# Optimization experiments

Hardware: AMD Instinct MI355X
Metric: run time of the kernel (lower is better)

The kernel has to match this reference:

```python
import jax, jax.numpy as jnp
import numpy as np

N = 40000; E = 500000; IN = 128; ED = 16; HID = 64; HEADS = 4; OUT = 256; B = 128
NEG = 0.2  # GATv2 leaky_relu negative slope


def _add_self_loops(edge_index, edge_attr, n):
    # PyG add_self_loops with fill_value='mean': loop attr = mean of incoming edge attrs per node
    dst = edge_index[1]
    s = jax.ops.segment_sum(edge_attr, dst, num_segments=n)
    c = jax.ops.segment_sum(jnp.ones((edge_attr.shape[0],), edge_attr.dtype), dst, num_segments=n)
    loop_attr = s / jnp.maximum(c, 1.0)[:, None]
    loops = jnp.arange(n, dtype=edge_index.dtype)
    ei = jnp.concatenate([edge_index, jnp.stack([loops, loops])], axis=1)
    ea = jnp.concatenate([edge_attr, loop_attr], axis=0)
    return ei, ea


def _seg_softmax(logits, seg, n):
    m = jax.ops.segment_max(logits, seg, num_segments=n)
    m = jnp.where(jnp.isfinite(m), m, 0.0)  # guard empty segments
    e = jnp.exp(logits - m[seg])
    z = jax.ops.segment_sum(e, seg, num_segments=n)
    return e / (z[seg] + 1e-16)


def _gatv2(x, src, dst, ea, Wl, bl, Wr, br, We, att, bias, heads, oc, concat):
    n = x.shape[0]
    xl = (x @ Wl + bl).reshape(n, heads, oc)  # lin_l (source/message transform)
    xr = (x @ Wr + br).reshape(n, heads, oc)  # lin_r (target transform)
    ef = (ea @ We).reshape(-1, heads, oc)     # lin_edge (no bias)
    s = jax.nn.leaky_relu(xl[src] + xr[dst] + ef, NEG)  # [Etot,H,C]
    alpha = _seg_softmax(jnp.einsum('ehc,hc->eh', s, att), dst, n)  # scatter-softmax over dst
    out = jax.ops.segment_sum(xl[src] * alpha[..., None], dst, num_segments=n)  # [N,H,C]
    out = out.reshape(n, heads * oc) if concat else out.mean(axis=1)
    return out + bias


def setup_inputs():
    ks = jax.random.split(jax.random.key(0), 32)
    W = lambda i, shp: jax.random.normal(ks[i], shp, jnp.float32) * 0.05
    z = lambda d: jnp.zeros((d,), jnp.float32)
    H = HEADS * HID
    return dict(
        x=jax.random.normal(ks[0], (N, IN), jnp.float32),
        edge_index=jax.random.randint(ks[1], (2, E), 0, N),
        edge_attr=jax.random.normal(ks[2], (E, ED), jnp.float32),
        batch=jnp.sort(jax.random.randint(ks[3], (N,), 0, B)),
        batch_size=B,
        c1_Wl=W(4, (IN, H)), c1_bl=z(H), c1_Wr=W(5, (IN, H)), c1_br=z(H), c1_We=W(6, (ED, H)), c1_att=W(7, (HEADS, HID)), c1_bias=z(H),
        c2_Wl=W(8, (H, H)), c2_bl=z(H), c2_Wr=W(9, (H, H)), c2_br=z(H), c2_We=W(10, (ED, H)), c2_att=W(11, (HEADS, HID)), c2_bias=z(H),
        c3_Wl=W(12, (H, OUT)), c3_bl=z(OUT), c3_Wr=W(13, (H, OUT)), c3_br=z(OUT), c3_We=W(14, (ED, OUT)), c3_att=W(15, (1, OUT)), c3_bias=z(OUT),
        gate_W1=W(16, (OUT, 128)), gate_b1=z(128), gate_W2=W(17, (128, 1)), gate_b2=z(1),
        reg_W1=W(18, (OUT, 128)), reg_b1=z(128), reg_W2=W(19, (128, 2)), reg_b2=z(2),
    )


def reference(x, edge_index, edge_attr, batch, batch_size,
              c1_Wl, c1_bl, c1_Wr, c1_br, c1_We, c1_att, c1_bias,
              c2_Wl, c2_bl, c2_Wr, c2_br, c2_We, c2_att, c2_bias,
              c3_Wl, c3_bl, c3_Wr, c3_br, c3_We, c3_att, c3_bias,
              gate_W1, gate_b1, gate_W2, gate_b2,
              reg_W1, reg_b1, reg_W2, reg_b2):
    # task_type='homo_lumo' path; dropout disabled (inference)
    ei, ea = _add_self_loops(edge_index, edge_attr, N)
    src, dst = ei[0], ei[1]
    h = jax.nn.relu(_gatv2(x, src, dst, ea, c1_Wl, c1_bl, c1_Wr, c1_br, c1_We, c1_att, c1_bias, HEADS, HID, True))
    h = jax.nn.relu(_gatv2(h, src, dst, ea, c2_Wl, c2_bl, c2_Wr, c2_br, c2_We, c2_att, c2_bias, HEADS, HID, True))
    h = _gatv2(h, src, dst, ea, c3_Wl, c3_bl, c3_Wr, c3_br, c3_We, c3_att, c3_bias, 1, OUT, True)
    # AttentionalAggregation pooling
    gate = jax.nn.relu(h @ gate_W1 + gate_b1) @ gate_W2 + gate_b2  # [N,1]
    a = _seg_softmax(gate[:, 0], batch, batch_size)
    g = jax.ops.segment_sum(h * a[:, None], batch, num_segments=batch_size)  # [B,OUT]
    return jax.nn.relu(g @ reg_W1 + reg_b1) @ reg_W2 + reg_b2  # [B,2]
```

## Files before the change

kernel.cpp:

```cpp
#include <hip/hip_runtime.h>
#include <math.h>

constexpr int N_NODES = 40000;
constexpr int N_EDGES = 500000;
constexpr int ETOT    = N_EDGES + N_NODES;
constexpr int IN_DIM  = 128;
constexpr int ED_DIM  = 16;
constexpr int FEAT    = 256;
constexpr int BATCH   = 128;
constexpr float NEG   = 0.2f;
constexpr int NCHUNK  = (N_NODES + 255) / 256;

__global__ __launch_bounds__(256) void k_deg(const int* __restrict__ dst, int* __restrict__ deg)
{
    int e = blockIdx.x * 256 + threadIdx.x;
    if (e >= ETOT) return;
    int v = e < N_EDGES ? dst[e] : e - N_EDGES;
    atomicAdd(&deg[v], 1);
}

__global__ __launch_bounds__(256) void k_scan1(const int* __restrict__ deg, int* __restrict__ bsum)
{
    __shared__ int s[256];
    int t = threadIdx.x;
    int idx = blockIdx.x * 256 + t;
    s[t] = idx < N_NODES ? deg[idx] : 0;
    __syncthreads();
    for (int st = 128; st; st >>= 1) { if (t < st) s[t] += s[t + st]; __syncthreads(); }
    if (t == 0) bsum[blockIdx.x] = s[0];
}

__global__ __launch_bounds__(256) void k_scan2(const int* __restrict__ bsum,
    int* __restrict__ boff, int* __restrict__ rowptr)
{
    __shared__ int s[256];
    int t = threadIdx.x;
    int v = t < NCHUNK ? bsum[t] : 0;
    s[t] = v;
    __syncthreads();
    for (int off = 1; off < 256; off <<= 1) {
        int x = (t >= off) ? s[t - off] : 0;
        __syncthreads();
        s[t] += x;
        __syncthreads();
    }
    if (t < NCHUNK) boff[t] = s[t] - v;
    if (t == 0) rowptr[N_NODES] = ETOT;
}

__global__ __launch_bounds__(256) void k_scan3(const int* __restrict__ deg,
    const int* __restrict__ boff, int* __restrict__ rowptr)
{
    __shared__ int s[256];
    int t = threadIdx.x;
    int idx = blockIdx.x * 256 + t;
    int v = idx < N_NODES ? deg[idx] : 0;
    s[t] = v;
    __syncthreads();
    for (int off = 1; off < 256; off <<= 1) {
        int x = (t >= off) ? s[t - off] : 0;
        __syncthreads();
        s[t] += x;
        __syncthreads();
    }
    if (idx < N_NODES) rowptr[idx] = boff[blockIdx.x] + s[t] - v;
}

__global__ __launch_bounds__(256) void k_fill(const int* __restrict__ srcA, const int* __restrict__ dst,
    const int* __restrict__ rowptr, int* __restrict__ fill, int2* __restrict__ elist2)
{
    int e = blockIdx.x * 256 + threadIdx.x;
    if (e >= ETOT) return;
    int v = e < N_EDGES ? dst[e]  : e - N_EDGES;
    int s = e < N_EDGES ? srcA[e] : e - N_EDGES;
    int pos = rowptr[v] + atomicAdd(&fill[v], 1);
    elist2[pos] = make_int2(s, e);
}

__global__ __launch_bounds__(256) void k_loop_csr(const int2* __restrict__ elist2,
    const int* __restrict__ rowptr, const float* __restrict__ ea, float* __restrict__ loop_attr)
{
    int t = blockIdx.x * 256 + threadIdx.x;
    if (t >= N_NODES * ED_DIM) return;
    int n = t >> 4, d = t & 15;
    int p0 = rowptr[n], p1 = rowptr[n + 1];
    float s = 0.f; int c = 0;
    for (int p = p0; p < p1; ++p) {
        int e = elist2[p].y;
        if (e < N_EDGES) { s += ea[(size_t)e * ED_DIM + d]; ++c; }
    }
    loop_attr[t] = s / (float)(c > 0 ? c : 1);
}

__global__ __launch_bounds__(256) void k_gemm(const float* __restrict__ A, const float* __restrict__ W,
    const float* __restrict__ bias, float* __restrict__ C, int M, int N, int K, int act)
{
    __shared__ float As[16][136];
    __shared__ float Bs[16][136];
    int t = threadIdx.x;
    int bm = blockIdx.x * 128, bn = blockIdx.y * 128;
    int tr = t >> 4, tc = t & 15;
    int mr0 = tr * 8, nc0 = tc * 4;

    float acc[8][8] = {};

    for (int k0 = 0; k0 < K; k0 += 16) {
        #pragma unroll
        for (int ii = 0; ii < 2; ++ii) {
            int i = t + ii * 256;
            int row = i >> 2, kq = (i & 3) << 2;
            int r = bm + row; r = r < M ? r : M - 1;
            float4 av = *(const float4*)(A + (size_t)r * K + k0 + kq);
            As[kq + 0][row] = av.x; As[kq + 1][row] = av.y;
            As[kq + 2][row] = av.z; As[kq + 3][row] = av.w;
        }
        #pragma unroll
        for (int ii = 0; ii < 2; ++ii) {
            int i = t + ii * 256;
            int krow = i >> 5, nq = (i & 31) << 2;
            float4 bv = *(const float4*)(W + (size_t)(k0 + krow) * N + bn + nq);
            *(float4*)&Bs[krow][nq] = bv;
        }
        __syncthreads();
        #pragma unroll
        for (int k = 0; k < 16; ++k) {
            float4 a0 = *(const float4*)&As[k][mr0];
            float4 a1 = *(const float4*)&As[k][mr0 + 4];
            float4 b0 = *(const float4*)&Bs[k][nc0];
            float4 b1 = *(const float4*)&Bs[k][64 + nc0];
            float am[8] = {a0.x, a0.y, a0.z, a0.w, a1.x, a1.y, a1.z, a1.w};
            float bv[8] = {b0.x, b0.y, b0.z, b0.w, b1.x, b1.y, b1.z, b1.w};
            #pragma unroll
            for (int i = 0; i < 8; ++i)
                #pragma unroll
                for (int j = 0; j < 8; ++j)
                    acc[i][j] = fmaf(am[i], bv[j], acc[i][j]);
        }
        __syncthreads();
    }

    float bb[8];
    #pragma unroll
    for (int j = 0; j < 4; ++j) { bb[j] = bias[bn + nc0 + j]; bb[j + 4] = bias[bn + 64 + nc0 + j]; }
    #pragma unroll
    for (int i = 0; i < 8; ++i) {
        int row = bm + mr0 + i;
        if (row >= M) break;
        float4 o0, o1;
        o0.x = acc[i][0] + bb[0]; o0.y = acc[i][1] + bb[1];
        o0.z = acc[i][2] + bb[2]; o0.w = acc[i][3] + bb[3];
        o1.x = acc[i][4] + bb[4]; o1.y = acc[i][5] + bb[5];
        o1.z = acc[i][6] + bb[6]; o1.w = acc[i][7] + bb[7];
        if (act) {
            o0.x = fmaxf(o0.x, 0.f); o0.y = fmaxf(o0.y, 0.f); o0.z = fmaxf(o0.z, 0.f); o0.w = fmaxf(o0.w, 0.f);
            o1.x = fmaxf(o1.x, 0.f); o1.y = fmaxf(o1.y, 0.f); o1.z = fmaxf(o1.z, 0.f); o1.w = fmaxf(o1.w, 0.f);
        }
        *(float4*)(C + (size_t)row * N + bn + nc0)      = o0;
        *(float4*)(C + (size_t)row * N + bn + 64 + nc0) = o1;
    }
}

static void launch_gemm(const float* A, const float* W, const float* bias, float* C,
                        int M, int N, int K, int act, hipStream_t stream)
{
    dim3 grid((M + 127) / 128, N / 128);
    k_gemm<<<grid, 256, 0, stream>>>(A, W, bias, C, M, N, K, act);
}


#define XELOAD(s) do {                                                                \
    int src_ = eS[s].x, e_ = eS[s].y;                                                 \
    const float4* eb4_ = reinterpret_cast<const float4*>(                             \
        (e_ < N_EDGES) ? ea + (size_t)e_ * ED_DIM                                     \
                       : loop_attr + (size_t)src_ * ED_DIM);                          \
    evS[s][0] = eb4_[0]; evS[s][1] = eb4_[1];                                         \
    evS[s][2] = eb4_[2]; evS[s][3] = eb4_[3];                                         \
    const float* xp_ = xl + (size_t)src_ * FEAT + base;                               \
    xlvS[s][0] = xp_[0];  xlvS[s][1] = xp_[16];                                       \
    xlvS[s][2] = xp_[32]; xlvS[s][3] = xp_[48];                                       \
} while (0)

#define COMPUTE(s) do {                                                               \
    float ef0_ = 0.f, ef1_ = 0.f, ef2_ = 0.f, ef3_ = 0.f;                             \
    const float* ed_ = (const float*)evS[s];                                          \
    _Pragma("unroll")                                                                 \
    for (int d_ = 0; d_ < ED_DIM; ++d_) {                                             \
        float a_ = ed_[d_];                                                           \
        ef0_ = fmaf(a_, weR[d_][0], ef0_); ef1_ = fmaf(a_, weR[d_][1], ef1_);         \
        ef2_ = fmaf(a_, weR[d_][2], ef2_); ef3_ = fmaf(a_, weR[d_][3], ef3_);         \
    }                                                                                 \
    float s0_ = xlvS[s][0] + xrv[0] + ef0_;                                           \
    float s1_ = xlvS[s][1] + xrv[1] + ef1_;                                           \
    float s2_ = xlvS[s][2] + xrv[2] + ef2_;                                           \
    float s3_ = xlvS[s][3] + xrv[3] + ef3_;                                           \
    s0_ = fmaxf(s0_, 0.f) + NEG * fminf(s0_, 0.f);                                    \
    s1_ = fmaxf(s1_, 0.f) + NEG * fminf(s1_, 0.f);                                    \
    s2_ = fmaxf(s2_, 0.f) + NEG * fminf(s2_, 0.f);                                    \
    s3_ = fmaxf(s3_, 0.f) + NEG * fminf(s3_, 0.f);                                    \
    float l_ = fmaf(s0_, attR[0], fmaf(s1_, attR[1], fmaf(s2_, attR[2], s3_ * attR[3])));\
    l_ += __shfl_xor(l_, 1, 64);                                                      \
    l_ += __shfl_xor(l_, 2, 64);                                                      \
    l_ += __shfl_xor(l_, 4, 64);                                                      \
    l_ += __shfl_xor(l_, 8, 64);                                                      \
    if (H == 1) { l_ += __shfl_xor(l_, 16, 64); l_ += __shfl_xor(l_, 32, 64); }       \
    float nm_ = fmaxf(m, l_);                                                         \
    float sc_ = __expf(m - nm_);                                                      \
    float w_  = __expf(l_ - nm_);                                                     \
    z = fmaf(z, sc_, w_);                                                             \
    m = nm_;                                                                          \
    acc[0] = fmaf(acc[0], sc_, w_ * xlvS[s][0]);                                      \
    acc[1] = fmaf(acc[1], sc_, w_ * xlvS[s][1]);                                      \
    acc[2] = fmaf(acc[2], sc_, w_ * xlvS[s][2]);                                      \
    acc[3] = fmaf(acc[3], sc_, w_ * xlvS[s][3]);                                      \
} while (0)

template <int H, int RELU>
__global__ __launch_bounds__(256, 3) void k_gat(
    const float* __restrict__ xl, const float* __restrict__ xr,
    const float* __restrict__ ea, const float* __restrict__ loop_attr,
    const int2* __restrict__ elist2, const int* __restrict__ rowptr,
    const float* __restrict__ We, const float* __restrict__ att,
    const float* __restrict__ bias, float* __restrict__ out)
{
    int t = threadIdx.x;
    int lane = t & 63;
    int n = __builtin_amdgcn_readfirstlane(blockIdx.x * 4 + (t >> 6));
    int q = lane >> 4;
    int u = lane & 15;
    int base = q * 64 + u;

    float weR[ED_DIM][4];
    #pragma unroll
    for (int d = 0; d < ED_DIM; ++d) {
        #pragma unroll
        for (int j = 0; j < 4; ++j) weR[d][j] = We[d * FEAT + base + 16 * j];
    }
    #pragma unroll
    for (int d = 0; d < ED_DIM; ++d) {
        #pragma unroll
        for (int j = 0; j < 4; ++j) asm volatile("" : "+v"(weR[d][j]));
    }

    float attR[4], xrv[4];
    #pragma unroll
    for (int j = 0; j < 4; ++j) {
        attR[j] = att[base + 16 * j];
        xrv[j]  = xr[(size_t)n * FEAT + base + 16 * j];
    }

    float m = -INFINITY, z = 0.f;
    float acc[4] = {0.f, 0.f, 0.f, 0.f};

    int p0 = rowptr[n], p1 = rowptr[n + 1];
    int pe = p1 - 1;

    int2   eS[2];
    float4 evS[2][4];
    float  xlvS[2][4];

    eS[0] = elist2[p0];
    { int pc = p0 + 1 > pe ? pe : p0 + 1; eS[1] = elist2[pc]; }
    XELOAD(0);

    int p = p0;
    while (true) {
        XELOAD(1);
        { int pn = p + 2 > pe ? pe : p + 2; eS[0] = elist2[pn]; }
        COMPUTE(0);
        if (++p >= p1) break;
        XELOAD(0);
        { int pn = p + 2 > pe ? pe : p + 2; eS[1] = elist2[pn]; }
        COMPUTE(1);
        if (++p >= p1) break;
    }

    float inv = 1.0f / (z + 1e-16f);
    #pragma unroll
    for (int j = 0; j < 4; ++j) {
        float o = fmaf(acc[j], inv, bias[base + 16 * j]);
        if (RELU) o = fmaxf(o, 0.f);
        out[(size_t)n * FEAT + base + 16 * j] = o;
    }
}

__global__ __launch_bounds__(256) void k_gate_score(const float* __restrict__ ghid,
    const float* __restrict__ W2, const float* __restrict__ b2, float* __restrict__ gate)
{
    int lane = threadIdx.x & 63;
    int n = blockIdx.x * 4 + (threadIdx.x >> 6);
    float v = ghid[(size_t)n * 128 + lane] * W2[lane] + ghid[(size_t)n * 128 + lane + 64] * W2[lane + 64];
    #pragma unroll
    for (int off = 32; off > 0; off >>= 1) v += __shfl_xor(v, off, 64);
    if (lane == 0) gate[n] = v + b2[0];
}

__device__ __forceinline__ int lbound(const int* a, int n, int v)
{
    int lo = 0, hi = n;
    while (lo < hi) { int mid = (lo + hi) >> 1; if (a[mid] < v) lo = mid + 1; else hi = mid; }
    return lo;
}

__global__ __launch_bounds__(256) void k_pool(const float* __restrict__ gate,
    const float* __restrict__ h, const int* __restrict__ batch, float* __restrict__ g)
{
    int b = blockIdx.x;
    int t = threadIdx.x;
    __shared__ float red[256];
    int start = lbound(batch, N_NODES, b);
    int end   = lbound(batch, N_NODES, b + 1);

    float mx = -INFINITY;
    for (int n = start + t; n < end; n += 256) mx = fmaxf(mx, gate[n]);
    red[t] = mx; __syncthreads();
    for (int s = 128; s; s >>= 1) { if (t < s) red[t] = fmaxf(red[t], red[t + s]); __syncthreads(); }
    float m = red[0];
    __syncthreads();

    float zs = 0.f;
    for (int n = start + t; n < end; n += 256) zs += __expf(gate[n] - m);
    red[t] = zs; __syncthreads();
    for (int s = 128; s; s >>= 1) { if (t < s) red[t] += red[t + s]; __syncthreads(); }
    float z = red[0];

    float gs = 0.f;
    for (int n = start; n < end; ++n) gs += __expf(gate[n] - m) * h[(size_t)n * FEAT + t];
    g[b * FEAT + t] = gs / (z + 1e-16f);
}

__global__ __launch_bounds__(128) void k_reg(const float* __restrict__ g,
    const float* __restrict__ W1, const float* __restrict__ b1,
    const float* __restrict__ W2, const float* __restrict__ b2, float* __restrict__ out)
{
    int b = blockIdx.x, t = threadIdx.x;
    __shared__ float sg[FEAT];
    sg[t] = g[b * FEAT + t];
    sg[t + 128] = g[b * FEAT + t + 128];
    __syncthreads();
    float hv = b1[t];
    for (int k = 0; k < FEAT; ++k) hv += sg[k] * W1[k * 128 + t];
    hv = fmaxf(hv, 0.f);
    __shared__ float p0s[128], p1s[128];
    p0s[t] = hv * W2[t * 2 + 0];
    p1s[t] = hv * W2[t * 2 + 1];
    __syncthreads();
    for (int s = 64; s; s >>= 1) {
        if (t < s) { p0s[t] += p0s[t + s]; p1s[t] += p1s[t + s]; }
        __syncthreads();
    }
    if (t == 0) { out[b * 2 + 0] = p0s[0] + b2[0]; out[b * 2 + 1] = p1s[0] + b2[1]; }
}

extern "C" void kernel_launch(void* const* d_in, const int* in_sizes, int n_in,
                              void* d_out, int out_size, void* d_ws, size_t ws_size,
                              hipStream_t stream)
{
    const float* x       = (const float*)d_in[0];
    const int*   ei      = (const int*)d_in[1];
    const float* ea      = (const float*)d_in[2];
    const int*   batch   = (const int*)d_in[3];
    const float* c1_Wl   = (const float*)d_in[5];
    const float* c1_bl   = (const float*)d_in[6];
    const float* c1_Wr   = (const float*)d_in[7];
    const float* c1_br   = (const float*)d_in[8];
    const float* c1_We   = (const float*)d_in[9];
    const float* c1_att  = (const float*)d_in[10];
    const float* c1_bias = (const float*)d_in[11];
    const float* c2_Wl   = (const float*)d_in[12];
    const float* c2_bl   = (const float*)d_in[13];
    const float* c2_Wr   = (const float*)d_in[14];
    const float* c2_br   = (const float*)d_in[15];
    const float* c2_We   = (const float*)d_in[16];
    const float* c2_att  = (const float*)d_in[17];
    const float* c2_bias = (const float*)d_in[18];
    const float* c3_Wl   = (const float*)d_in[19];
    const float* c3_bl   = (const float*)d_in[20];
    const float* c3_Wr   = (const float*)d_in[21];
    const float* c3_br   = (const float*)d_in[22];
    const float* c3_We   = (const float*)d_in[23];
    const float* c3_att  = (const float*)d_in[24];
    const float* c3_bias = (const float*)d_in[25];
    const float* gate_W1 = (const float*)d_in[26];
    const float* gate_b1 = (const float*)d_in[27];
    const float* gate_W2 = (const float*)d_in[28];
    const float* gate_b2 = (const float*)d_in[29];
    const float* reg_W1  = (const float*)d_in[30];
    const float* reg_b1  = (const float*)d_in[31];
    const float* reg_W2  = (const float*)d_in[32];
    const float* reg_b2  = (const float*)d_in[33];

    const int* srcArr = ei;
    const int* dstArr = ei + N_EDGES;

    float* ws = (float*)d_ws;
    size_t off = 0;
    auto alloc = [&](size_t nf) { float* p = ws + off; off += (nf + 63) & ~(size_t)63; return p; };
    float* xl        = alloc((size_t)N_NODES * FEAT);
    float* xr        = alloc((size_t)N_NODES * FEAT);
    float* h         = alloc((size_t)N_NODES * FEAT);
    float* loop_attr = alloc((size_t)N_NODES * ED_DIM);
    float* gpool     = alloc((size_t)BATCH * FEAT);
    int* ibase  = (int*)(ws + off);
    int* deg    = ibase;
    int* fill   = ibase + N_NODES;
    int* rowptr = ibase + 2 * N_NODES;
    int* bsum   = ibase + 3 * N_NODES + 64;
    int* boff   = bsum + 256;
    int2* elist2 = (int2*)(boff + 256);

    float* ghid = xl;
    float* gate = xr;

    hipMemsetAsync(deg, 0, (size_t)2 * N_NODES * sizeof(int), stream);

    k_deg<<<(ETOT + 255) / 256, 256, 0, stream>>>(dstArr, deg);
    k_scan1<<<NCHUNK, 256, 0, stream>>>(deg, bsum);
    k_scan2<<<1, 256, 0, stream>>>(bsum, boff, rowptr);
    k_scan3<<<NCHUNK, 256, 0, stream>>>(deg, boff, rowptr);
    k_fill<<<(ETOT + 255) / 256, 256, 0, stream>>>(srcArr, dstArr, rowptr, fill, elist2);
    k_loop_csr<<<(N_NODES * ED_DIM + 255) / 256, 256, 0, stream>>>(elist2, rowptr, ea, loop_attr);

    launch_gemm(x, c1_Wl, c1_bl, xl, N_NODES, FEAT, IN_DIM, 0, stream);
    launch_gemm(x, c1_Wr, c1_br, xr, N_NODES, FEAT, IN_DIM, 0, stream);
    k_gat<4, 1><<<N_NODES / 4, 256, 0, stream>>>(xl, xr, ea, loop_attr, elist2, rowptr,
                                                 c1_We, c1_att, c1_bias, h);
    launch_gemm(h, c2_Wl, c2_bl, xl, N_NODES, FEAT, FEAT, 0, stream);
    launch_gemm(h, c2_Wr, c2_br, xr, N_NODES, FEAT, FEAT, 0, stream);
    k_gat<4, 1><<<N_NODES / 4, 256, 0, stream>>>(xl, xr, ea, loop_attr, elist2, rowptr,
                                                 c2_We, c2_att, c2_bias, h);
    launch_gemm(h, c3_Wl, c3_bl, xl, N_NODES, FEAT, FEAT, 0, stream);
    launch_gemm(h, c3_Wr, c3_br, xr, N_NODES, FEAT, FEAT, 0, stream);
    k_gat<1, 0><<<N_NODES / 4, 256, 0, stream>>>(xl, xr, ea, loop_attr, elist2, rowptr,
                                                 c3_We, c3_att, c3_bias, h);

    launch_gemm(h, gate_W1, gate_b1, ghid, N_NODES, 128, FEAT, 1, stream);
    k_gate_score<<<N_NODES / 4, 256, 0, stream>>>(ghid, gate_W2, gate_b2, gate);
    k_pool<<<BATCH, 256, 0, stream>>>(gate, h, batch, gpool);
    k_reg<<<BATCH, 128, 0, stream>>>(gpool, reg_W1, reg_b1, reg_W2, reg_b2, (float*)d_out);
}
```

Measured before the change: 1.216 ms.

## Register-prefetch next GEMM tile and pin edge weights as vector registers

The GEMM now loads the next K-slice of A and W into registers while computing on the current shared-memory tile, turning the load/compute sequence into a software pipeline with one fewer barrier per iteration. Each thread's A load is reorganized to two contiguous float4s per row. In the GAT kernel, the per-thread edge-weight slice is held in four 16-wide vector registers and pinned with an asm barrier inside the edge loop, so the compiler keeps them resident rather than rematerializing or spilling them. Costs are more live registers in the GEMM, which may reduce occupancy.

```diff
diff --git a/kernel.cpp b/kernel.cpp
--- a/kernel.cpp
+++ b/kernel.cpp
@@ -11,6 +11,8 @@
 constexpr float NEG   = 0.2f;
 constexpr int NCHUNK  = (N_NODES + 255) / 256;
 
+typedef float vfloat16 __attribute__((ext_vector_type(16)));
+
 __global__ __launch_bounds__(256) void k_deg(const int* __restrict__ dst, int* __restrict__ deg)
 {
     int e = blockIdx.x * 256 + threadIdx.x;
@@ -102,26 +104,32 @@
     int tr = t >> 4, tc = t & 15;
     int mr0 = tr * 8, nc0 = tc * 4;
 
+    int ar0 = t >> 1,        ak0 = (t & 1) << 3;
+    int bk0 = t >> 5,        bn0 = (t & 31) << 2;
+
     float acc[8][8] = {};
 
+    int r0 = bm + ar0; r0 = r0 < M ? r0 : M - 1;
+    float4 avA = *(const float4*)(A + (size_t)r0 * K + ak0);
+    float4 avB = *(const float4*)(A + (size_t)r0 * K + ak0 + 4);
+    float4 bvA = *(const float4*)(W + (size_t)bk0 * N + bn + bn0);
+    float4 bvB = *(const float4*)(W + (size_t)(bk0 + 8) * N + bn + bn0);
+
     for (int k0 = 0; k0 < K; k0 += 16) {
-        #pragma unroll
-        for (int ii = 0; ii < 2; ++ii) {
-            int i = t + ii * 256;
-            int row = i >> 2, kq = (i & 3) << 2;
-            int r = bm + row; r = r < M ? r : M - 1;
-            float4 av = *(const float4*)(A + (size_t)r * K + k0 + kq);
-            As[kq + 0][row] = av.x; As[kq + 1][row] = av.y;
-            As[kq + 2][row] = av.z; As[kq + 3][row] = av.w;
+        __syncthreads();
+        As[ak0 + 0][ar0] = avA.x; As[ak0 + 1][ar0] = avA.y;
+        As[ak0 + 2][ar0] = avA.z; As[ak0 + 3][ar0] = avA.w;
+        As[ak0 + 4][ar0] = avB.x; As[ak0 + 5][ar0] = avB.y;
+        As[ak0 + 6][ar0] = avB.z; As[ak0 + 7][ar0] = avB.w;
+        *(float4*)&Bs[bk0][bn0]     = bvA;
+        *(float4*)&Bs[bk0 + 8][bn0] = bvB;
+        __syncthreads();
+        if (k0 + 16 < K) {
+            avA = *(const float4*)(A + (size_t)r0 * K + k0 + 16 + ak0);
+            avB = *(const float4*)(A + (size_t)r0 * K + k0 + 16 + ak0 + 4);
+            bvA = *(const float4*)(W + (size_t)(k0 + 16 + bk0) * N + bn + bn0);
+            bvB = *(const float4*)(W + (size_t)(k0 + 24 + bk0) * N + bn + bn0);
         }
-        #pragma unroll
-        for (int ii = 0; ii < 2; ++ii) {
-            int i = t + ii * 256;
-            int krow = i >> 5, nq = (i & 31) << 2;
-            float4 bv = *(const float4*)(W + (size_t)(k0 + krow) * N + bn + nq);
-            *(float4*)&Bs[krow][nq] = bv;
-        }
-        __syncthreads();
         #pragma unroll
         for (int k = 0; k < 16; ++k) {
             float4 a0 = *(const float4*)&As[k][mr0];
@@ -136,7 +144,6 @@
                 for (int j = 0; j < 8; ++j)
                     acc[i][j] = fmaf(am[i], bv[j], acc[i][j]);
         }
-        __syncthreads();
     }
 
     float bb[8];
@@ -186,8 +193,8 @@
     _Pragma("unroll")                                                                 \
     for (int d_ = 0; d_ < ED_DIM; ++d_) {                                             \
         float a_ = ed_[d_];                                                           \
-        ef0_ = fmaf(a_, weR[d_][0], ef0_); ef1_ = fmaf(a_, weR[d_][1], ef1_);         \
-        ef2_ = fmaf(a_, weR[d_][2], ef2_); ef3_ = fmaf(a_, weR[d_][3], ef3_);         \
+        ef0_ = fmaf(a_, weV0[d_], ef0_); ef1_ = fmaf(a_, weV1[d_], ef1_);             \
+        ef2_ = fmaf(a_, weV2[d_], ef2_); ef3_ = fmaf(a_, weV3[d_], ef3_);             \
     }                                                                                 \
     float s0_ = xlvS[s][0] + xrv[0] + ef0_;                                           \
     float s1_ = xlvS[s][1] + xrv[1] + ef1_;                                           \
@@ -214,6 +221,8 @@
     acc[3] = fmaf(acc[3], sc_, w_ * xlvS[s][3]);                                      \
 } while (0)
 
+#define PIN_WE() asm volatile("" : "+v"(weV0), "+v"(weV1), "+v"(weV2), "+v"(weV3))
+
 template <int H, int RELU>
 __global__ __launch_bounds__(256, 3) void k_gat(
     const float* __restrict__ xl, const float* __restrict__ xr,
@@ -229,17 +238,15 @@
     int u = lane & 15;
     int base = q * 64 + u;
 
-    float weR[ED_DIM][4];
+    vfloat16 weV0, weV1, weV2, weV3;
     #pragma unroll
     for (int d = 0; d < ED_DIM; ++d) {
-        #pragma unroll
-        for (int j = 0; j < 4; ++j) weR[d][j] = We[d * FEAT + base + 16 * j];
-    }
-    #pragma unroll
-    for (int d = 0; d < ED_DIM; ++d) {
-        #pragma unroll
-        for (int j = 0; j < 4; ++j) asm volatile("" : "+v"(weR[d][j]));
-    }
+        weV0[d] = We[d * FEAT + base];
+        weV1[d] = We[d * FEAT + base + 16];
+        weV2[d] = We[d * FEAT + base + 32];
+        weV3[d] = We[d * FEAT + base + 48];
+    }
+    PIN_WE();
 
     float attR[4], xrv[4];
     #pragma unroll
@@ -264,6 +271,7 @@
 
     int p = p0;
     while (true) {
+        PIN_WE();
         XELOAD(1);
         { int pn = p + 2 > pe ? pe : p + 2; eS[0] = elist2[pn]; }
         COMPUTE(0);
```

New measurement: 1.223 ms. Within noise of the previous version (+0.6%).
